# Optimization experiments

Measured on AMD Instinct MI355X. Metric: run time of the kernel, lower is better.

The kernel has to match this reference:

```python
import jax, jax.numpy as jnp
import numpy as np

N_PATCHES = 14
PS = 16            # patch size: 224 / 14
C, H_IMG, W_IMG = 3, 224, 224
HIDDEN = 768
HEADS = 12
DH = HIDDEN // HEADS
BLOCKS = 12
MLP = 4 * HIDDEN
OUT = 1000
SEQ = N_PATCHES ** 2 + 1  # 197
BATCH = 64


def get_positional_embeddings(seq_len, d):
    # sin(i/10000^(j/d)) for even j, cos(i/10000^((j-1)/d)) for odd j
    i = jnp.arange(seq_len, dtype=jnp.float32)[:, None]
    j = jnp.arange(d)[None, :]
    even = (j % 2 == 0)
    expo = jnp.where(even, j, j - 1).astype(jnp.float32) / d
    ang = i / (10000.0 ** expo)
    return jnp.where(even, jnp.sin(ang), jnp.cos(ang))


def layernorm(x, g, b, eps=1e-5):
    mu = x.mean(-1, keepdims=True)
    var = ((x - mu) ** 2).mean(-1, keepdims=True)
    return (x - mu) / jnp.sqrt(var + eps) * g + b


def mhsa(x, qw, qb, kw, kb, vw, vb):
    # x: [B,S,HIDDEN]; per-head linears qw/kw/vw: [H,DH,DH] (torch Linear weight layout)
    B, S, _ = x.shape
    xh = x.reshape(B, S, HEADS, DH)
    q = jnp.einsum('bshd,hed->bshe', xh, qw) + qb
    k = jnp.einsum('bshd,hed->bshe', xh, kw) + kb
    v = jnp.einsum('bshd,hed->bshe', xh, vw) + vb
    scores = jnp.einsum('bshe,bthe->bhst', q, k) / jnp.sqrt(jnp.float32(DH))
    attn = jax.nn.softmax(scores, axis=-1)
    out = jnp.einsum('bhst,bthe->bshe', attn, v)
    return out.reshape(B, S, HIDDEN)


def vit_block(x, p):
    ln1_g, ln1_b, qw, qb, kw, kb, vw, vb, ln2_g, ln2_b, w1, b1, w2, b2 = p
    x = x + mhsa(layernorm(x, ln1_g, ln1_b), qw, qb, kw, kb, vw, vb)
    h = layernorm(x, ln2_g, ln2_b)
    h = jax.nn.gelu(h @ w1.T + b1, approximate=False) @ w2.T + b2
    return x + h


def patchify(images):
    # [N,C,H,W] -> [N, n_patches^2, C*PS*PS], channel-major within each patch
    n = images.shape[0]
    x = images.reshape(n, C, N_PATCHES, PS, N_PATCHES, PS)
    x = x.transpose(0, 2, 4, 1, 3, 5)  # n, pi, pj, c, ps, ps
    return x.reshape(n, N_PATCHES * N_PATCHES, C * PS * PS)


def setup_inputs() -> dict:
    key = jax.random.key(0)
    ks = jax.random.split(key, 20)
    s = 0.02
    return {
        'images': jax.random.normal(ks[0], (BATCH, C, H_IMG, W_IMG), jnp.float32),
        'mapper_w': jax.random.normal(ks[1], (HIDDEN, C * PS * PS), jnp.float32) * s,
        'mapper_b': jnp.zeros((HIDDEN,), jnp.float32),
        'cls_token': jax.random.uniform(ks[2], (1, HIDDEN), jnp.float32),
        'ln1_g': jnp.ones((BLOCKS, HIDDEN), jnp.float32),
        'ln1_b': jnp.zeros((BLOCKS, HIDDEN), jnp.float32),
        'qw': jax.random.normal(ks[3], (BLOCKS, HEADS, DH, DH), jnp.float32) * s,
        'qb': jnp.zeros((BLOCKS, HEADS, DH), jnp.float32),
        'kw': jax.random.normal(ks[4], (BLOCKS, HEADS, DH, DH), jnp.float32) * s,
        'kb': jnp.zeros((BLOCKS, HEADS, DH), jnp.float32),
        'vw': jax.random.normal(ks[5], (BLOCKS, HEADS, DH, DH), jnp.float32) * s,
        'vb': jnp.zeros((BLOCKS, HEADS, DH), jnp.float32),
        'ln2_g': jnp.ones((BLOCKS, HIDDEN), jnp.float32),
        'ln2_b': jnp.zeros((BLOCKS, HIDDEN), jnp.float32),
        'w1': jax.random.normal(ks[6], (BLOCKS, MLP, HIDDEN), jnp.float32) * s,
        'b1': jnp.zeros((BLOCKS, MLP), jnp.float32),
        'w2': jax.random.normal(ks[7], (BLOCKS, HIDDEN, MLP), jnp.float32) * s,
        'b2': jnp.zeros((BLOCKS, HIDDEN), jnp.float32),
        'head_w': jax.random.normal(ks[8], (OUT, HIDDEN), jnp.float32) * s,
        'head_b': jnp.zeros((OUT,), jnp.float32),
    }


def reference(images, mapper_w, mapper_b, cls_token, ln1_g, ln1_b, qw, qb, kw, kb,
              vw, vb, ln2_g, ln2_b, w1, b1, w2, b2, head_w, head_b):
    n = images.shape[0]
    patches = patchify(images)
    tokens = patches @ mapper_w.T + mapper_b                      # [B, 196, HIDDEN]
    cls = jnp.broadcast_to(cls_token[None], (n, 1, HIDDEN))
    tokens = jnp.concatenate([cls, tokens], axis=1)               # [B, 197, HIDDEN]
    out = tokens + get_positional_embeddings(SEQ, HIDDEN)[None]

    stacked = (ln1_g, ln1_b, qw, qb, kw, kb, vw, vb, ln2_g, ln2_b, w1, b1, w2, b2)

    def step(x, p):
        return vit_block(x, p), None

    out, _ = jax.lax.scan(step, out, stacked)
    cls_out = out[:, 0]                                           # [B, HIDDEN]
    return jax.nn.softmax(cls_out @ head_w.T + head_b, axis=-1)
```

## Files before the change

kernel.cpp:

```cpp
#include <hip/hip_runtime.h>
#include <cstdint>
#include <cstddef>
#include <cstdio>

using u16 = unsigned short;
using u32 = unsigned int;

typedef __attribute__((ext_vector_type(8))) __bf16 bf16x8;
typedef __attribute__((ext_vector_type(4))) float f32x4;

struct alignas(16) U128 { u32 w[4]; };
struct alignas(16) F4   { float x[4]; };
struct alignas(8)  US4  { u16 h[4]; };

#define DEVFN static __device__ __forceinline__

DEVFN u16 f2bf(float x) {
  union { float f; u32 u; } v; v.f = x;
  u32 r = v.u + 0x7fffu + ((v.u >> 16) & 1u);
  return (u16)(r >> 16);
}

DEVFN bf16x8 ld16(const u16* p) { return __builtin_bit_cast(bf16x8, *(const U128*)p); }

DEVFN f32x4 mfma16(bf16x8 a, bf16x8 b, f32x4 c) {
  return __builtin_amdgcn_mfma_f32_16x16x32_bf16(a, b, c, 0, 0, 0);
}

DEVFN void gload_lds16(const u16* g, u16* l) {
  __builtin_amdgcn_global_load_lds(
      (const __attribute__((address_space(1))) void*)g,
      (__attribute__((address_space(3))) void*)l, 16, 0, 0);
}

DEVFN float gelu(float x) {
  float z = fabsf(x) * 0.70710678118f;
  float t = __builtin_amdgcn_rcpf(1.f + 0.3275911f * z);
  float p = t * (0.254829592f + t * (-0.284496736f + t * (1.421413741f +
            t * (-1.453152027f + t * 1.061405429f))));
  float e = __expf(-z * z);
  float erfz = 1.f - p * e;
  erfz = copysignf(erfz, x);
  return 0.5f * x * (1.f + erfz);
}

DEVFN void remap_bid(int bid, int Mb, int Nb, int& bm, int& bn) {
  const int ngrp  = Mb >> 3;
  const int per   = Nb << 3;
  const int nfull = ngrp * per;
  if (bid < nfull) {
    const int bmg = bid / per;
    const int rem = bid - bmg * per;
    bn = rem >> 3;
    bm = (bmg << 3) + (rem & 7);
  } else {
    const int r = bid - nfull;
    const int q = r / Nb;
    bm = (ngrp << 3) + q;
    bn = r - q * Nb;
  }
}

constexpr int SEQL   = 197;
constexpr int NB     = 64;
constexpr int NH     = 12;
constexpr int MROWS  = NB * SEQL;
constexpr int MPAD   = 12672;
constexpr int MPAD2  = 12800;
constexpr int MPATCH = NB * 196;
constexpr int SP     = 208;
constexpr int SP2    = 224;
constexpr int BHN    = NB * NH;

constexpr int QSZ    = 2304 * 128;
constexpr int WSZ    = 3072 * 768;

constexpr size_t OFF_X    = 0;
constexpr size_t OFF_ALN  = OFF_X    + (size_t)MPAD * 768 * 4;
constexpr size_t OFF_H    = OFF_ALN  + (size_t)MPAD2 * 768 * 2;
constexpr size_t OFF_WMAP = OFF_H    + (size_t)MPAD2 * 3072 * 2;
constexpr size_t OFF_Q    = OFF_WMAP + (size_t)768 * 768 * 2;
constexpr size_t OFF_K    = OFF_Q    + (size_t)BHN * SP * 64 * 2;
constexpr size_t OFF_VT   = OFF_K    + (size_t)BHN * SP * 64 * 2;
constexpr size_t OFF_PAT  = OFF_VT   + (size_t)BHN * 64 * SP2 * 2;
constexpr size_t OFF_POS  = OFF_PAT  + (size_t)MPATCH * 768 * 2;
constexpr size_t OFF_WTS  = OFF_POS  + (size_t)SEQL * 768 * 4;
constexpr size_t WS_SMALL = OFF_WTS + (size_t)(QSZ + 2 * WSZ) * 2;
constexpr size_t WS_BIG   = OFF_WTS + (size_t)12 * (QSZ + 2 * WSZ) * 2;

__global__ void zero_kernel(u32* __restrict__ p, long n) {
  long i = (long)blockIdx.x * 256 + threadIdx.x;
  long stride = (long)gridDim.x * 256;
  for (; i < n; i += stride) p[i] = 0u;
}

__global__ void padzero_kernel(u16* __restrict__ Q, u16* __restrict__ Kp,
                               u16* __restrict__ Vt) {
  const int NQ32 = BHN * 352;
  const int NV   = BHN * 64 * 27;
  int i = blockIdx.x * 256 + threadIdx.x;
  if (i < NQ32) {
    int bh = i / 352, r = i - bh * 352;
    ((u32*)(Q + ((size_t)bh * SP + 197) * 64))[r] = 0u;
  } else if (i < 2 * NQ32) {
    int j = i - NQ32;
    int bh = j / 352, r = j - bh * 352;
    ((u32*)(Kp + ((size_t)bh * SP + 197) * 64))[r] = 0u;
  } else if (i < 2 * NQ32 + NV) {
    int j = i - 2 * NQ32;
    int be = j / 27, s = j - be * 27;
    Vt[(size_t)be * SP2 + 197 + s] = 0;
  }
}

__global__ void cvt_kernel(const float* __restrict__ src, u16* __restrict__ dst, int n) {
  int i = blockIdx.x * 256 + threadIdx.x;
  if (i < n) dst[i] = f2bf(src[i]);
}

__global__ void pos_kernel(float* __restrict__ pos) {
  int i = blockIdx.x * 256 + threadIdx.x;
  if (i >= SEQL * 768) return;
  int s = i / 768, j = i - s * 768;
  float expo = (float)(j & ~1) * (1.0f / 768.0f);
  float ang  = (float)s * expf(-expo * logf(10000.0f));
  pos[i] = (j & 1) ? cosf(ang) : sinf(ang);
}

__global__ void cls_kernel(const float* __restrict__ cls, const float* __restrict__ pos,
                           float* __restrict__ X) {
  int b = blockIdx.x;
  for (int c = threadIdx.x; c < 768; c += 256)
    X[(size_t)b * SEQL * 768 + c] = cls[c] + pos[c];
}

__global__ void patchify_kernel(const float* __restrict__ img, u16* __restrict__ out) {
  int i = blockIdx.x * 256 + threadIdx.x;
  if (i >= MPATCH * 768) return;
  int m = i / 768, k = i - m * 768;
  int b = m / 196, p = m - b * 196;
  int py = p / 14, px = p - py * 14;
  int c = k >> 8, rem = k & 255, iy = rem >> 4, ix = rem & 15;
  float v = img[(((size_t)b * 3 + c) * 224 + py * 16 + iy) * 224 + px * 16 + ix];
  out[i] = f2bf(v);
}

__global__ void prep_all(const float* __restrict__ qw, const float* __restrict__ kw,
                         const float* __restrict__ vw, const float* __restrict__ w1,
                         const float* __restrict__ w2,
                         u16* __restrict__ Wq, u16* __restrict__ W1b,
                         u16* __restrict__ W2b) {
  const int NQ = 12 * QSZ;
  const int NV = 12 * (WSZ / 4);
  int i = blockIdx.x * 256 + threadIdx.x;
  if (i < NQ) {
    int blk = i / QSZ;
    int r = i - blk * QSZ;
    int n = r >> 7, kk = r & 127;
    int p = n / 768, ef = n - p * 768;
    int h = ef >> 6, e = ef & 63;
    float v = 0.f;
    if ((kk >> 6) == (h & 1)) {
      int d = kk & 63;
      const float* w = (p == 0) ? qw : (p == 1) ? kw : vw;
      v = w[(((size_t)blk * NH + h) * 64 + e) * 64 + d];
    }
    Wq[i] = f2bf(v);
  } else if (i < NQ + NV) {
    int j = (i - NQ) * 4;
    F4 v = *(const F4*)(w1 + j);
    US4 o;
    #pragma unroll
    for (int r = 0; r < 4; ++r) o.h[r] = f2bf(v.x[r]);
    *(US4*)(W1b + j) = o;
  } else if (i < NQ + 2 * NV) {
    int j = (i - NQ - NV) * 4;
    F4 v = *(const F4*)(w2 + j);
    US4 o;
    #pragma unroll
    for (int r = 0; r < 4; ++r) o.h[r] = f2bf(v.x[r]);
    *(US4*)(W2b + j) = o;
  }
}

__global__ void prep_kernel(const float* __restrict__ qw, const float* __restrict__ kw,
                            const float* __restrict__ vw, const float* __restrict__ w1,
                            const float* __restrict__ w2,
                            u16* __restrict__ Wqkv, u16* __restrict__ W1b,
                            u16* __restrict__ W2b, int blk) {
  const int NV = WSZ / 4;
  int i = blockIdx.x * 256 + threadIdx.x;
  if (i < QSZ) {
    int n = i >> 7, kk = i & 127;
    int p = n / 768, ef = n - p * 768;
    int h = ef >> 6, e = ef & 63;
    float v = 0.f;
    if ((kk >> 6) == (h & 1)) {
      int d = kk & 63;
      const float* w = (p == 0) ? qw : (p == 1) ? kw : vw;
      v = w[(((size_t)blk * NH + h) * 64 + e) * 64 + d];
    }
    Wqkv[i] = f2bf(v);
  } else if (i < QSZ + NV) {
    int j = (i - QSZ) * 4;
    F4 v = *(const F4*)(w1 + (size_t)blk * WSZ + j);
    US4 o;
    #pragma unroll
    for (int r = 0; r < 4; ++r) o.h[r] = f2bf(v.x[r]);
    *(US4*)(W1b + j) = o;
  } else if (i < QSZ + 2 * NV) {
    int j = (i - QSZ - NV) * 4;
    F4 v = *(const F4*)(w2 + (size_t)blk * WSZ + j);
    US4 o;
    #pragma unroll
    for (int r = 0; r < 4; ++r) o.h[r] = f2bf(v.x[r]);
    *(US4*)(W2b + j) = o;
  }
}

__global__ __launch_bounds__(256) void ln_kernel(const float* __restrict__ X,
    const float* __restrict__ g, const float* __restrict__ b, u16* __restrict__ out) {
  int row  = blockIdx.x * 4 + (threadIdx.x >> 6);
  int lane = threadIdx.x & 63;
  const float* x = X + (size_t)row * 768 + lane * 12;
  F4 a0 = *(const F4*)(x);
  F4 a1 = *(const F4*)(x + 4);
  F4 a2 = *(const F4*)(x + 8);
  float v[12];
  #pragma unroll
  for (int j = 0; j < 4; ++j) { v[j] = a0.x[j]; v[4 + j] = a1.x[j]; v[8 + j] = a2.x[j]; }
  float s = 0.f, q = 0.f;
  #pragma unroll
  for (int j = 0; j < 12; ++j) { s += v[j]; q += v[j] * v[j]; }
  #pragma unroll
  for (int d = 1; d < 64; d <<= 1) { s += __shfl_xor(s, d); q += __shfl_xor(q, d); }
  float mu  = s * (1.f / 768.f);
  float var = q * (1.f / 768.f) - mu * mu;
  float rs  = rsqrtf(var + 1e-5f);
  const float* gp = g + lane * 12;
  const float* bp = b + lane * 12;
  u16* op = out + (size_t)row * 768 + lane * 12;
  u16 o[12];
  #pragma unroll
  for (int j = 0; j < 12; ++j) o[j] = f2bf((v[j] - mu) * rs * gp[j] + bp[j]);
  #pragma unroll
  for (int c = 0; c < 3; ++c) {
    US4 w; w.h[0] = o[c*4]; w.h[1] = o[c*4+1]; w.h[2] = o[c*4+2]; w.h[3] = o[c*4+3];
    *(US4*)(op + c * 4) = w;
  }
}

enum { EPI_PATCH = 0, EPI_QKV = 1, EPI_GELU = 2, EPI_RESID = 3 };

template<int EPI>
__global__ __launch_bounds__(256, 3) void gemm128(
    const u16* __restrict__ A, const u16* __restrict__ B, int K, int lda, int ldb,
    int Mb, int Nb,
    const float* __restrict__ e0, const float* __restrict__ e1, const float* __restrict__ e2,
    float* __restrict__ f0, const float* __restrict__ f1,
    u16* __restrict__ o0, u16* __restrict__ o1, u16* __restrict__ o2) {
  __shared__ u16 Ab[3][128 * 32];
  __shared__ u16 Bb[3][128 * 32];
  const int tid  = threadIdx.x;
  const int wave = tid >> 6, lane = tid & 63;
  int bm, bn;
  remap_bid(blockIdx.x, Mb, Nb, bm, bn);
  const int fr = lane & 15, fg = lane >> 4;
  const int srow = wave * 16 + (lane >> 2);
  const int gcol = ((lane & 3) ^ ((lane >> 3) & 3)) * 8;
  const u16* gA = A + (size_t)(bm * 128 + srow) * lda + gcol;
  const u16* gB = B + (size_t)(bn * 128 + srow) * ldb + gcol;
  const int wm = (wave >> 1) * 64, wn = (wave & 1) * 64;
  const int sl = (fg ^ ((fr >> 1) & 3)) * 8;
  const int nt = K >> 5;

  auto STAGE = [&](int c, int t) {
    gload_lds16(gA + t * 32,                    &Ab[c][0] + wave * 512);
    gload_lds16(gA + t * 32 + (size_t)64 * lda, &Ab[c][0] + wave * 512 + 2048);
    gload_lds16(gB + t * 32,                    &Bb[c][0] + wave * 512);
    gload_lds16(gB + t * 32 + (size_t)64 * ldb, &Bb[c][0] + wave * 512 + 2048);
  };

  f32x4 acc[4][4] = {};
  STAGE(0, 0);
  if (nt > 1) STAGE(1, 1);
  int bi = 0;
  for (int t = 0; t < nt; ++t) {
    if (t + 1 < nt) asm volatile("s_waitcnt vmcnt(4)" ::: "memory");
    else            asm volatile("s_waitcnt vmcnt(0)" ::: "memory");
    __builtin_amdgcn_s_barrier();
    if (t + 2 < nt) { int si = bi + 2; if (si >= 3) si -= 3; STAGE(si, t + 2); }
    const u16* ab   = &Ab[bi][0];
    const u16* bbuf = &Bb[bi][0];
    bf16x8 af[4], bfv[4];
    #pragma unroll
    for (int i = 0; i < 4; ++i) af[i]  = ld16(ab + (wm + i * 16 + fr) * 32 + sl);
    #pragma unroll
    for (int j = 0; j < 4; ++j) bfv[j] = ld16(bbuf + (wn + j * 16 + fr) * 32 + sl);
    __builtin_amdgcn_s_setprio(1);
    #pragma unroll
    for (int i = 0; i < 4; ++i)
      #pragma unroll
      for (int j = 0; j < 4; ++j)
        acc[i][j] = mfma16(af[i], bfv[j], acc[i][j]);
    __builtin_amdgcn_s_setprio(0);
    bi = (bi + 1 == 3) ? 0 : bi + 1;
  }

  #pragma unroll
  for (int i = 0; i < 4; ++i) {
    #pragma unroll
    for (int r = 0; r < 4; ++r) {
      const int m = bm * 128 + wm + i * 16 + fg * 4 + r;
      if constexpr (EPI == EPI_PATCH) {
        const int bb = m / 196;
        const int s  = m - bb * 196 + 1;
        float* xrow = f0 + ((size_t)bb * SEQL + s) * 768;
        const float* prow = f1 + (size_t)s * 768;
        #pragma unroll
        for (int j = 0; j < 4; ++j) {
          const int n = bn * 128 + wn + j * 16 + fr;
          xrow[n] = acc[i][j][r] + e0[n] + prow[n];
        }
      } else {
        if (m < MROWS) {
          float* xrow = f0 + (size_t)m * 768;
          #pragma unroll
          for (int j = 0; j < 4; ++j) {
            const int n = bn * 128 + wn + j * 16 + fr;
            xrow[n] += acc[i][j][r] + e0[n];
          }
        }
      }
    }
  }
}

__global__ __launch_bounds__(256, 3) void gemm128f_gelu(
    const u16* __restrict__ A, const u16* __restrict__ B,
    const float* __restrict__ e0, u16* __restrict__ o0,
    int ntiles, int nblocks) {
  __shared__ u16 Ab[3][128 * 32];
  __shared__ u16 Bb[3][128 * 32];
  constexpr int lda = 768, ldb = 768, nt = 24;
  const int tid = threadIdx.x, wave = tid >> 6, lane = tid & 63;
  const int fr = lane & 15, fg = lane >> 4;
  const int srow = wave * 16 + (lane >> 2);
  const int gcol = ((lane & 3) ^ ((lane >> 3) & 3)) * 8;
  const int wm = (wave >> 1) * 64, wn = (wave & 1) * 64;
  const int sl = (fg ^ ((fr >> 1) & 3)) * 8;
  const int myTiles = (ntiles - (int)blockIdx.x + nblocks - 1) / nblocks;
  const int total = myTiles * nt;

  int s_t  = blockIdx.x;
  int s_kk = 0;
  const u16 *s_gA, *s_gB;
  {
    int bm, bn; remap_bid(s_t, 99, 24, bm, bn);
    s_gA = A + (size_t)(bm * 128 + srow) * lda + gcol;
    s_gB = B + (size_t)(bn * 128 + srow) * ldb + gcol;
  }
  auto STAGE1 = [&](int c) {
    gload_lds16(s_gA + s_kk * 32,                    &Ab[c][0] + wave * 512);
    gload_lds16(s_gA + s_kk * 32 + (size_t)64 * lda, &Ab[c][0] + wave * 512 + 2048);
    gload_lds16(s_gB + s_kk * 32,                    &Bb[c][0] + wave * 512);
    gload_lds16(s_gB + s_kk * 32 + (size_t)64 * ldb, &Bb[c][0] + wave * 512 + 2048);
    if (++s_kk == nt) {
      s_kk = 0;
      s_t += nblocks;
      if (s_t < ntiles) {
        int bm, bn; remap_bid(s_t, 99, 24, bm, bn);
        s_gA = A + (size_t)(bm * 128 + srow) * lda + gcol;
        s_gB = B + (size_t)(bn * 128 + srow) * ldb + gcol;
      }
    }
  };

  STAGE1(0);
  if (total > 1) STAGE1(1);
  int bi = 0, g = 0;
  for (int t = blockIdx.x; t < ntiles; t += nblocks) {
    int bm, bn; remap_bid(t, 99, 24, bm, bn);
    f32x4 acc[4][4] = {};
    for (int k = 0; k < nt; ++k, ++g) {
      if (g + 1 < total) asm volatile("s_waitcnt vmcnt(4)" ::: "memory");
      else               asm volatile("s_waitcnt vmcnt(0)" ::: "memory");
      __builtin_amdgcn_s_barrier();
      if (g + 2 < total) { int si = bi + 2; if (si >= 3) si -= 3; STAGE1(si); }
      const u16* ab   = &Ab[bi][0];
      const u16* bbuf = &Bb[bi][0];
      bf16x8 af[4], bfv[4];
      #pragma unroll
      for (int i = 0; i < 4; ++i) af[i]  = ld16(ab + (wm + i * 16 + fr) * 32 + sl);
      #pragma unroll
      for (int j = 0; j < 4; ++j) bfv[j] = ld16(bbuf + (wn + j * 16 + fr) * 32 + sl);
      __builtin_amdgcn_s_setprio(1);
      #pragma unroll
      for (int i = 0; i < 4; ++i)
        #pragma unroll
        for (int j = 0; j < 4; ++j)
          acc[i][j] = mfma16(af[i], bfv[j], acc[i][j]);
      __builtin_amdgcn_s_setprio(0);
      bi = (bi + 1 == 3) ? 0 : bi + 1;
    }
    #pragma unroll
    for (int i = 0; i < 4; ++i) {
      #pragma unroll
      for (int r = 0; r < 4; ++r) {
        const int m = bm * 128 + wm + i * 16 + fg * 4 + r;
        u16* hrow = o0 + (size_t)m * 3072;
        #pragma unroll
        for (int j = 0; j < 4; ++j) {
          const int n = bn * 128 + wn + j * 16 + fr;
          hrow[n] = f2bf(gelu(acc[i][j][r] + e0[n]));
        }
      }
    }
  }
}

__global__ __launch_bounds__(256, 2) void qkv_gemm(
    const u16* __restrict__ A, const u16* __restrict__ B,
    const float* __restrict__ e0, const float* __restrict__ e1, const float* __restrict__ e2,
    u16* __restrict__ o0, u16* __restrict__ o1, u16* __restrict__ o2) {
  __shared__ u16 Ab[4][128 * 32];
  __shared__ u16 Bb[4][128 * 32];
  const int tid = threadIdx.x, wave = tid >> 6, lane = tid & 63;
  int bm, bn;
  remap_bid(blockIdx.x, MPAD / 128, 18, bm, bn);
  const int fr = lane & 15, fg = lane >> 4;
  const u16* Aw = A + (bn % 6) * 128;
  const int srow = wave * 16 + (lane >> 2);
  const int gcol = ((lane & 3) ^ ((lane >> 3) & 3)) * 8;
  const u16* gA = Aw + (size_t)(bm * 128 + srow) * 768 + gcol;
  const u16* gB = B + (size_t)(bn * 128 + srow) * 128 + gcol;
  const int wm = (wave >> 1) * 64, wn = (wave & 1) * 64;
  const int sl = (fg ^ ((fr >> 1) & 3)) * 8;

  #pragma unroll
  for (int c = 0; c < 4; ++c) {
    gload_lds16(gA + c * 32,                    &Ab[c][0] + wave * 512);
    gload_lds16(gA + c * 32 + (size_t)64 * 768, &Ab[c][0] + wave * 512 + 2048);
    gload_lds16(gB + c * 32,                    &Bb[c][0] + wave * 512);
    gload_lds16(gB + c * 32 + (size_t)64 * 128, &Bb[c][0] + wave * 512 + 2048);
  }
  asm volatile("s_waitcnt vmcnt(0)" ::: "memory");
  __builtin_amdgcn_s_barrier();

  f32x4 acc[4][4] = {};
  #pragma unroll
  for (int c = 0; c < 4; ++c) {
    bf16x8 af[4], bfv[4];
    #pragma unroll
    for (int i = 0; i < 4; ++i) af[i]  = ld16(&Ab[c][0] + (wm + i * 16 + fr) * 32 + sl);
    #pragma unroll
    for (int j = 0; j < 4; ++j) bfv[j] = ld16(&Bb[c][0] + (wn + j * 16 + fr) * 32 + sl);
    __builtin_amdgcn_s_setprio(1);
    #pragma unroll
    for (int i = 0; i < 4; ++i)
      #pragma unroll
      for (int j = 0; j < 4; ++j)
        acc[i][j] = mfma16(af[i], bfv[j], acc[i][j]);
    __builtin_amdgcn_s_setprio(0);
  }

  #pragma unroll
  for (int i = 0; i < 4; ++i) {
    #pragma unroll
    for (int r = 0; r < 4; ++r) {
      const int m = bm * 128 + wm + i * 16 + fg * 4 + r;
      if (m < MROWS) {
        const int bb = m / 197;
        const int s  = m - bb * 197;
        #pragma unroll
        for (int j = 0; j < 4; ++j) {
          const int n = bn * 128 + wn + j * 16 + fr;
          const int p = n / 768;
          const int ef = n - p * 768;
          const int h = ef >> 6, e = ef & 63;
          const size_t bh = (size_t)bb * NH + h;
          if (p == 0)      o0[(bh * SP + s) * 64 + e] = f2bf((acc[i][j][r] + e0[ef]) * 0.125f);
          else if (p == 1) o1[(bh * SP + s) * 64 + e] = f2bf(acc[i][j][r] + e1[ef]);
          else             o2[(bh * 64 + e) * SP2 + s] = f2bf(acc[i][j][r] + e2[ef]);
        }
      }
    }
  }
}

__global__ __launch_bounds__(256, 2) void attn_kernel(const u16* __restrict__ Q,
    const u16* __restrict__ Km, const u16* __restrict__ Vt, float* __restrict__ X) {
  __shared__ u16  P[4][16 * SP2];
  __shared__ u16  Kl[208 * 72];
  __shared__ float sums[4][16];
  const int bh = blockIdx.x;
  const int b = bh / NH, h = bh - b * NH;
  const int wave = threadIdx.x >> 6, lane = threadIdx.x & 63;
  const int fr = lane & 15, fg = lane >> 4;
  const u16* Qb = Q  + (size_t)bh * SP * 64;
  const u16* Kb = Km + (size_t)bh * SP * 64;
  const u16* Vb = Vt + (size_t)bh * 64 * SP2;
  {
    const int r0 = threadIdx.x >> 2;
    const int e  = (threadIdx.x & 3) * 16;
    #pragma unroll
    for (int rr = r0; rr < 208; rr += 64)
      *(U128*)(Kl + rr * 72 + e) = *(const U128*)(Kb + (size_t)rr * 64 + e);
  }
  __syncthreads();
  u16* Pl = &P[wave][0];
  for (int qt = wave; qt < 13; qt += 4) {
    const int s0 = qt * 16;
    bf16x8 qf0 = ld16(Qb + (size_t)(s0 + fr) * 64 + fg * 8);
    bf16x8 qf1 = ld16(Qb + (size_t)(s0 + fr) * 64 + 32 + fg * 8);
    f32x4 sc[13];
    #pragma unroll
    for (int tf = 0; tf < 13; ++tf) {
      f32x4 a = {0.f, 0.f, 0.f, 0.f};
      bf16x8 k0 = ld16(Kl + (tf * 16 + fr) * 72 + fg * 8);
      bf16x8 k1 = ld16(Kl + (tf * 16 + fr) * 72 + 32 + fg * 8);
      a = mfma16(qf0, k0, a);
      a = mfma16(qf1, k1, a);
      sc[tf] = a;
    }
    float mx[4] = {-3e38f, -3e38f, -3e38f, -3e38f};
    #pragma unroll
    for (int tf = 0; tf < 13; ++tf) {
      const bool ok = (tf * 16 + fr) < 197;
      #pragma unroll
      for (int r = 0; r < 4; ++r) {
        float v = ok ? sc[tf][r] : -3e38f;
        sc[tf][r] = v;
        mx[r] = fmaxf(mx[r], v);
      }
    }
    #pragma unroll
    for (int r = 0; r < 4; ++r)
      #pragma unroll
      for (int d = 1; d < 16; d <<= 1) mx[r] = fmaxf(mx[r], __shfl_xor(mx[r], d));
    float sm[4] = {0.f, 0.f, 0.f, 0.f};
    #pragma unroll
    for (int tf = 0; tf < 13; ++tf) {
      #pragma unroll
      for (int r = 0; r < 4; ++r) {
        float e = __expf(sc[tf][r] - mx[r]);
        sm[r] += e;
        Pl[(fg * 4 + r) * SP2 + tf * 16 + fr] = f2bf(e);
      }
    }
    #pragma unroll
    for (int r = 0; r < 4; ++r) {
      #pragma unroll
      for (int d = 1; d < 16; d <<= 1) sm[r] += __shfl_xor(sm[r], d);
      if (fr == 0) sums[wave][fg * 4 + r] = sm[r];
    }
    #pragma unroll
    for (int r = 0; r < 4; ++r) Pl[(fg * 4 + r) * SP2 + 208 + fr] = 0;
    f32x4 o[4] = {};
    #pragma unroll
    for (int ks = 0; ks < 7; ++ks) {
      bf16x8 pf = ld16(Pl + fr * SP2 + ks * 32 + fg * 8);
      #pragma unroll
      for (int ef = 0; ef < 4; ++ef) {
        bf16x8 vf = ld16(Vb + (size_t)(ef * 16 + fr) * SP2 + ks * 32 + fg * 8);
        o[ef] = mfma16(vf, pf, o[ef]);
      }
    }
    const float inv = 1.f / sums[wave][fr];
    const int s = s0 + fr;
    if (s < 197) {
      float* xp = X + ((size_t)b * SEQL + s) * 768 + h * 64;
      #pragma unroll
      for (int ef = 0; ef < 4; ++ef)
        #pragma unroll
        for (int r = 0; r < 4; ++r)
          xp[ef * 16 + fg * 4 + r] += o[ef][r] * inv;
    }
  }
}

__global__ __launch_bounds__(256) void head_kernel(const float* __restrict__ X,
    const float* __restrict__ hw, const float* __restrict__ hb, float* __restrict__ out) {
  __shared__ float xr[768];
  __shared__ float lg[1000];
  __shared__ float red[8];
  const int b = blockIdx.x, tid = threadIdx.x;
  for (int c = tid; c < 768; c += 256) xr[c] = X[(size_t)b * SEQL * 768 + c];
  __syncthreads();
  for (int n = tid; n < 1000; n += 256) {
    const F4* w4 = (const F4*)(hw + (size_t)n * 768);
    const F4* x4 = (const F4*)xr;
    float acc = hb[n];
    for (int k = 0; k < 192; ++k) {
      F4 w = w4[k]; F4 xv = x4[k];
      acc += w.x[0] * xv.x[0] + w.x[1] * xv.x[1] + w.x[2] * xv.x[2] + w.x[3] * xv.x[3];
    }
    lg[n] = acc;
  }
  __syncthreads();
  float m = -3e38f;
  for (int n = tid; n < 1000; n += 256) m = fmaxf(m, lg[n]);
  #pragma unroll
  for (int d = 1; d < 64; d <<= 1) m = fmaxf(m, __shfl_xor(m, d));
  if ((tid & 63) == 0) red[tid >> 6] = m;
  __syncthreads();
  m = fmaxf(fmaxf(red[0], red[1]), fmaxf(red[2], red[3]));
  float s = 0.f;
  for (int n = tid; n < 1000; n += 256) s += expf(lg[n] - m);
  #pragma unroll
  for (int d = 1; d < 64; d <<= 1) s += __shfl_xor(s, d);
  if ((tid & 63) == 0) red[4 + (tid >> 6)] = s;
  __syncthreads();
  s = red[4] + red[5] + red[6] + red[7];
  const float inv = 1.f / s;
  for (int n = tid; n < 1000; n += 256) out[(size_t)b * 1000 + n] = expf(lg[n] - m) * inv;
}

extern "C" void kernel_launch(void* const* d_in, const int* in_sizes, int n_in,
                              void* d_out, int out_size, void* d_ws, size_t ws_size,
                              hipStream_t stream) {
  (void)in_sizes; (void)n_in; (void)out_size;
  if (ws_size < WS_SMALL) { printf("ws too small: %zu < %zu\n", ws_size, WS_SMALL); return; }
  const bool hoist = ws_size >= WS_BIG;

  const float* images   = (const float*)d_in[0];
  const float* mapper_w = (const float*)d_in[1];
  const float* mapper_b = (const float*)d_in[2];
  const float* cls_tok  = (const float*)d_in[3];
  const float* ln1_g    = (const float*)d_in[4];
  const float* ln1_b    = (const float*)d_in[5];
  const float* qw       = (const float*)d_in[6];
  const float* qb       = (const float*)d_in[7];
  const float* kw       = (const float*)d_in[8];
  const float* kb       = (const float*)d_in[9];
  const float* vw       = (const float*)d_in[10];
  const float* vb       = (const float*)d_in[11];
  const float* ln2_g    = (const float*)d_in[12];
  const float* ln2_b    = (const float*)d_in[13];
  const float* w1       = (const float*)d_in[14];
  const float* b1       = (const float*)d_in[15];
  const float* w2       = (const float*)d_in[16];
  const float* b2       = (const float*)d_in[17];
  const float* head_w   = (const float*)d_in[18];
  const float* head_b   = (const float*)d_in[19];

  char* ws = (char*)d_ws;
  float* X    = (float*)(ws + OFF_X);
  u16*  Aln   = (u16*)(ws + OFF_ALN);
  u16*  Hb    = (u16*)(ws + OFF_H);
  u16*  Wmap  = (u16*)(ws + OFF_WMAP);
  u16*  Qb    = (u16*)(ws + OFF_Q);
  u16*  Kb    = (u16*)(ws + OFF_K);
  u16*  Vtb   = (u16*)(ws + OFF_VT);
  u16*  Pat   = (u16*)(ws + OFF_PAT);
  float* Pos  = (float*)(ws + OFF_POS);
  u16*  WqA   = (u16*)(ws + OFF_WTS);
  u16*  W1A   = WqA + (size_t)(hoist ? 12 : 1) * QSZ;
  u16*  W2A   = W1A + (size_t)(hoist ? 12 : 1) * WSZ;

  padzero_kernel<<<(2 * BHN * 352 + BHN * 64 * 27 + 255) / 256, 256, 0, stream>>>(Qb, Kb, Vtb);
  zero_kernel<<<64, 256, 0, stream>>>((u32*)(X + (size_t)MROWS * 768), (long)((MPAD - MROWS) * 768));

  pos_kernel<<<(SEQL * 768 + 255) / 256, 256, 0, stream>>>(Pos);
  cvt_kernel<<<(768 * 768 + 255) / 256, 256, 0, stream>>>(mapper_w, Wmap, 768 * 768);
  patchify_kernel<<<(MPATCH * 768 + 255) / 256, 256, 0, stream>>>(images, Pat);
  cls_kernel<<<NB, 256, 0, stream>>>(cls_tok, Pos, X);

  if (hoist) {
    const int N_ALL = 12 * QSZ + 2 * 12 * (WSZ / 4);
    prep_all<<<(N_ALL + 255) / 256, 256, 0, stream>>>(qw, kw, vw, w1, w2, WqA, W1A, W2A);
  }

  gemm128<EPI_PATCH><<<(MPATCH / 128) * (768 / 128), 256, 0, stream>>>(
      Pat, Wmap, 768, 768, 768, MPATCH / 128, 768 / 128,
      mapper_b, nullptr, nullptr, X, Pos, nullptr, nullptr, nullptr);

  const int PREP_N = QSZ + 2 * (WSZ / 4);
  for (int blk = 0; blk < 12; ++blk) {
    u16* Wq_b = WqA + (size_t)(hoist ? blk : 0) * QSZ;
    u16* W1_b = W1A + (size_t)(hoist ? blk : 0) * WSZ;
    u16* W2_b = W2A + (size_t)(hoist ? blk : 0) * WSZ;
    ln_kernel<<<MPAD / 4, 256, 0, stream>>>(X, ln1_g + blk * 768, ln1_b + blk * 768, Aln);
    if (!hoist)
      prep_kernel<<<(PREP_N + 255) / 256, 256, 0, stream>>>(
          qw, kw, vw, w1, w2, Wq_b, W1_b, W2_b, blk);
    qkv_gemm<<<(MPAD / 128) * 18, 256, 0, stream>>>(
        Aln, Wq_b, qb + blk * 768, kb + blk * 768, vb + blk * 768, Qb, Kb, Vtb);
    attn_kernel<<<BHN, 256, 0, stream>>>(Qb, Kb, Vtb, X);
    ln_kernel<<<MPAD / 4, 256, 0, stream>>>(X, ln2_g + blk * 768, ln2_b + blk * 768, Aln);
    gemm128f_gelu<<<768, 256, 0, stream>>>(Aln, W1_b, b1 + blk * 3072, Hb, 2376, 768);
    gemm128<EPI_RESID><<<(MPAD / 128) * (768 / 128), 256, 0, stream>>>(
        Hb, W2_b, 3072, 3072, 3072, MPAD / 128, 768 / 128,
        b2 + blk * 768, nullptr, nullptr, X, nullptr, nullptr, nullptr, nullptr);
  }

  head_kernel<<<NB, 256, 0, stream>>>(X, head_w, head_b, (float*)d_out);
}
```

Measured before the change: 4.107 ms.

## Make QKV GEMM persistent with triple-buffered cross-tile pipelined loads

The per-tile QKV GEMM, which loaded all four K-chunks and then computed, becomes a persistent kernel over 768 blocks. Each block walks several output tiles, and a 3-stage LDS ring prefetches chunks across tile boundaries so global loads overlap MFMA work and epilogue stores. LDS use drops from 4 to 3 buffers per operand and launch bounds rise to 3 blocks per CU for occupancy. The cost is more barriers per tile and a fixed grid that may leave some blocks with an uneven number of tiles.

```diff
diff --git a/kernel.cpp b/kernel.cpp
--- a/kernel.cpp
+++ b/kernel.cpp
@@ -419,69 +419,95 @@
   }
 }
 
-__global__ __launch_bounds__(256, 2) void qkv_gemm(
+__global__ __launch_bounds__(256, 3) void qkv_flat(
     const u16* __restrict__ A, const u16* __restrict__ B,
     const float* __restrict__ e0, const float* __restrict__ e1, const float* __restrict__ e2,
-    u16* __restrict__ o0, u16* __restrict__ o1, u16* __restrict__ o2) {
-  __shared__ u16 Ab[4][128 * 32];
-  __shared__ u16 Bb[4][128 * 32];
+    u16* __restrict__ o0, u16* __restrict__ o1, u16* __restrict__ o2,
+    int ntiles, int nblocks) {
+  __shared__ u16 Ab[3][128 * 32];
+  __shared__ u16 Bb[3][128 * 32];
+  constexpr int lda = 768, ldb = 128, nt = 4;
   const int tid = threadIdx.x, wave = tid >> 6, lane = tid & 63;
-  int bm, bn;
-  remap_bid(blockIdx.x, MPAD / 128, 18, bm, bn);
   const int fr = lane & 15, fg = lane >> 4;
-  const u16* Aw = A + (bn % 6) * 128;
   const int srow = wave * 16 + (lane >> 2);
   const int gcol = ((lane & 3) ^ ((lane >> 3) & 3)) * 8;
-  const u16* gA = Aw + (size_t)(bm * 128 + srow) * 768 + gcol;
-  const u16* gB = B + (size_t)(bn * 128 + srow) * 128 + gcol;
   const int wm = (wave >> 1) * 64, wn = (wave & 1) * 64;
   const int sl = (fg ^ ((fr >> 1) & 3)) * 8;
-
-  #pragma unroll
-  for (int c = 0; c < 4; ++c) {
-    gload_lds16(gA + c * 32,                    &Ab[c][0] + wave * 512);
-    gload_lds16(gA + c * 32 + (size_t)64 * 768, &Ab[c][0] + wave * 512 + 2048);
-    gload_lds16(gB + c * 32,                    &Bb[c][0] + wave * 512);
-    gload_lds16(gB + c * 32 + (size_t)64 * 128, &Bb[c][0] + wave * 512 + 2048);
-  }
-  asm volatile("s_waitcnt vmcnt(0)" ::: "memory");
-  __builtin_amdgcn_s_barrier();
-
-  f32x4 acc[4][4] = {};
-  #pragma unroll
-  for (int c = 0; c < 4; ++c) {
-    bf16x8 af[4], bfv[4];
-    #pragma unroll
-    for (int i = 0; i < 4; ++i) af[i]  = ld16(&Ab[c][0] + (wm + i * 16 + fr) * 32 + sl);
-    #pragma unroll
-    for (int j = 0; j < 4; ++j) bfv[j] = ld16(&Bb[c][0] + (wn + j * 16 + fr) * 32 + sl);
-    __builtin_amdgcn_s_setprio(1);
-    #pragma unroll
-    for (int i = 0; i < 4; ++i)
-      #pragma unroll
-      for (int j = 0; j < 4; ++j)
-        acc[i][j] = mfma16(af[i], bfv[j], acc[i][j]);
-    __builtin_amdgcn_s_setprio(0);
-  }
-
-  #pragma unroll
-  for (int i = 0; i < 4; ++i) {
-    #pragma unroll
-    for (int r = 0; r < 4; ++r) {
-      const int m = bm * 128 + wm + i * 16 + fg * 4 + r;
-      if (m < MROWS) {
-        const int bb = m / 197;
-        const int s  = m - bb * 197;
+  const int myTiles = (ntiles - (int)blockIdx.x + nblocks - 1) / nblocks;
+  if (myTiles <= 0) return;
+  const int total = myTiles * nt;
+
+  int s_t  = blockIdx.x;
+  int s_kk = 0;
+  const u16 *s_gA, *s_gB;
+  {
+    int bm, bn; remap_bid(s_t, 99, 18, bm, bn);
+    s_gA = A + (bn % 6) * 128 + (size_t)(bm * 128 + srow) * lda + gcol;
+    s_gB = B + (size_t)(bn * 128 + srow) * ldb + gcol;
+  }
+  auto STAGE1 = [&](int c) {
+    gload_lds16(s_gA + s_kk * 32,                    &Ab[c][0] + wave * 512);
+    gload_lds16(s_gA + s_kk * 32 + (size_t)64 * lda, &Ab[c][0] + wave * 512 + 2048);
+    gload_lds16(s_gB + s_kk * 32,                    &Bb[c][0] + wave * 512);
+    gload_lds16(s_gB + s_kk * 32 + (size_t)64 * ldb, &Bb[c][0] + wave * 512 + 2048);
+    if (++s_kk == nt) {
+      s_kk = 0;
+      s_t += nblocks;
+      if (s_t < ntiles) {
+        int bm, bn; remap_bid(s_t, 99, 18, bm, bn);
+        s_gA = A + (bn % 6) * 128 + (size_t)(bm * 128 + srow) * lda + gcol;
+        s_gB = B + (size_t)(bn * 128 + srow) * ldb + gcol;
+      }
+    }
+  };
+
+  STAGE1(0);
+  if (total > 1) STAGE1(1);
+  int bi = 0, g = 0;
+  for (int t = blockIdx.x; t < ntiles; t += nblocks) {
+    int bm, bn; remap_bid(t, 99, 18, bm, bn);
+    f32x4 acc[4][4] = {};
+    #pragma unroll
+    for (int k = 0; k < nt; ++k, ++g) {
+      if (g + 1 < total) asm volatile("s_waitcnt vmcnt(4)" ::: "memory");
+      else               asm volatile("s_waitcnt vmcnt(0)" ::: "memory");
+      __builtin_amdgcn_s_barrier();
+      if (g + 2 < total) { int si = bi + 2; if (si >= 3) si -= 3; STAGE1(si); }
+      const u16* ab   = &Ab[bi][0];
+      const u16* bbuf = &Bb[bi][0];
+      bf16x8 af[4], bfv[4];
+      #pragma unroll
+      for (int i = 0; i < 4; ++i) af[i]  = ld16(ab + (wm + i * 16 + fr) * 32 + sl);
+      #pragma unroll
+      for (int j = 0; j < 4; ++j) bfv[j] = ld16(bbuf + (wn + j * 16 + fr) * 32 + sl);
+      __builtin_amdgcn_s_setprio(1);
+      #pragma unroll
+      for (int i = 0; i < 4; ++i)
         #pragma unroll
-        for (int j = 0; j < 4; ++j) {
-          const int n = bn * 128 + wn + j * 16 + fr;
-          const int p = n / 768;
-          const int ef = n - p * 768;
-          const int h = ef >> 6, e = ef & 63;
-          const size_t bh = (size_t)bb * NH + h;
-          if (p == 0)      o0[(bh * SP + s) * 64 + e] = f2bf((acc[i][j][r] + e0[ef]) * 0.125f);
-          else if (p == 1) o1[(bh * SP + s) * 64 + e] = f2bf(acc[i][j][r] + e1[ef]);
-          else             o2[(bh * 64 + e) * SP2 + s] = f2bf(acc[i][j][r] + e2[ef]);
+        for (int j = 0; j < 4; ++j)
+          acc[i][j] = mfma16(af[i], bfv[j], acc[i][j]);
+      __builtin_amdgcn_s_setprio(0);
+      bi = (bi + 1 == 3) ? 0 : bi + 1;
+    }
+    #pragma unroll
+    for (int i = 0; i < 4; ++i) {
+      #pragma unroll
+      for (int r = 0; r < 4; ++r) {
+        const int m = bm * 128 + wm + i * 16 + fg * 4 + r;
+        if (m < MROWS) {
+          const int bb = m / 197;
+          const int s  = m - bb * 197;
+          #pragma unroll
+          for (int j = 0; j < 4; ++j) {
+            const int n = bn * 128 + wn + j * 16 + fr;
+            const int p = n / 768;
+            const int ef = n - p * 768;
+            const int h = ef >> 6, e = ef & 63;
+            const size_t bh = (size_t)bb * NH + h;
+            if (p == 0)      o0[(bh * SP + s) * 64 + e] = f2bf((acc[i][j][r] + e0[ef]) * 0.125f);
+            else if (p == 1) o1[(bh * SP + s) * 64 + e] = f2bf(acc[i][j][r] + e1[ef]);
+            else             o2[(bh * 64 + e) * SP2 + s] = f2bf(acc[i][j][r] + e2[ef]);
+          }
         }
       }
     }
@@ -684,8 +710,9 @@
     if (!hoist)
       prep_kernel<<<(PREP_N + 255) / 256, 256, 0, stream>>>(
           qw, kw, vw, w1, w2, Wq_b, W1_b, W2_b, blk);
-    qkv_gemm<<<(MPAD / 128) * 18, 256, 0, stream>>>(
-        Aln, Wq_b, qb + blk * 768, kb + blk * 768, vb + blk * 768, Qb, Kb, Vtb);
+    qkv_flat<<<768, 256, 0, stream>>>(
+        Aln, Wq_b, qb + blk * 768, kb + blk * 768, vb + blk * 768,
+        Qb, Kb, Vtb, (MPAD / 128) * 18, 768);
     attn_kernel<<<BHN, 256, 0, stream>>>(Qb, Kb, Vtb, X);
     ln_kernel<<<MPAD / 4, 256, 0, stream>>>(X, ln2_g + blk * 768, ln2_b + blk * 768, Aln);
     gemm128f_gelu<<<768, 256, 0, stream>>>(Aln, W1_b, b1 + blk * 3072, Hb, 2376, 768);
```

After: 3.959 ms (median of 3 runs). -3.6%, faster.

## Use 256x256 tiled 8-wave GEMM for MLP layers and persistent QKV GEMM

Applied to the files above, without the earlier changes.

Replaces the 128x128 MLP GEMMs (FC1 with GELU, FC2 with residual) with a new 256x256-tile, 512-thread kernel using K=64 double-buffered LDS. Loads for the next stage are interleaved between four MFMA phases separated by barriers. The QKV projection becomes a persistent, triple-buffered kernel reusing the old flat-GELU pipeline. The goal is higher arithmetic intensity and better latency hiding. In exchange it needs a larger M padding (MPAD2) with extra zeroing of Aln and Hb rows, and fewer blocks for the small FC2 GEMM.

```diff
diff --git a/kernel.cpp b/kernel.cpp
--- a/kernel.cpp
+++ b/kernel.cpp
@@ -336,13 +336,129 @@
   }
 }
 
-__global__ __launch_bounds__(256, 3) void gemm128f_gelu(
+template<int MG, int KK>
+DEVFN void phase_mfma(const u16* ab, const u16* bbuf, int wr, int wc, int fr, int fg,
+                      f32x4 (&acc)[8][4], bf16x8 (&bf)[4], bool loadB) {
+  bf16x8 af[4];
+  #pragma unroll
+  for (int a = 0; a < 4; ++a) {
+    const int row = wr * 128 + (MG * 4 + a) * 16 + fr;
+    af[a] = ld16(ab + row * 64 + (((KK * 4 + fg) ^ (row & 7)) * 8));
+  }
+  if (loadB) {
+    #pragma unroll
+    for (int nf = 0; nf < 4; ++nf) {
+      const int row = wc * 64 + nf * 16 + fr;
+      bf[nf] = ld16(bbuf + row * 64 + (((KK * 4 + fg) ^ (row & 7)) * 8));
+    }
+  }
+  __builtin_amdgcn_s_setprio(1);
+  #pragma unroll
+  for (int a = 0; a < 4; ++a)
+    #pragma unroll
+    for (int nf = 0; nf < 4; ++nf)
+      acc[MG * 4 + a][nf] = mfma16(af[a], bf[nf], acc[MG * 4 + a][nf]);
+  __builtin_amdgcn_s_setprio(0);
+}
+
+template<int EPI>
+__global__ __launch_bounds__(512, 2) void gemm256p(
+    const u16* __restrict__ A, const u16* __restrict__ B, int K, int Mb, int Nb,
+    const float* __restrict__ e0, float* __restrict__ f0, u16* __restrict__ o0) {
+  __shared__ u16 Ab[2][256 * 64];
+  __shared__ u16 Bb[2][256 * 64];
+  const int tid = threadIdx.x;
+  const int wid = tid >> 6, lane = tid & 63;
+  const int fr = lane & 15, fg = lane >> 4;
+  const int wr = wid >> 2, wc = wid & 3;
+  int bm, bn;
+  remap_bid(blockIdx.x, Mb, Nb, bm, bn);
+  const int nt = K >> 6;
+
+  const int r0 = tid >> 3,        c0 = tid & 7;
+  const int r1 = (512 + tid) >> 3, c1 = (512 + tid) & 7;
+  const int gc0 = ((c0 ^ (r0 & 7)) * 8);
+  const int gc1 = ((c1 ^ (r1 & 7)) * 8);
+  const int d0 = (wid * 64) * 8;
+  const int d1 = (512 + wid * 64) * 8;
+
+  auto STAGE_A = [&](int b_, int h, int t) {
+    const u16* g0 = A + (size_t)(bm * 256 + h * 128 + r0) * K + t * 64 + gc0;
+    const u16* g1 = A + (size_t)(bm * 256 + h * 128 + r1) * K + t * 64 + gc1;
+    u16* base = &Ab[b_][0] + h * 8192;
+    gload_lds16(g0, base + d0);
+    gload_lds16(g1, base + d1);
+  };
+  auto STAGE_B = [&](int b_, int h, int t) {
+    const u16* g0 = B + (size_t)(bn * 256 + h * 128 + r0) * K + t * 64 + gc0;
+    const u16* g1 = B + (size_t)(bn * 256 + h * 128 + r1) * K + t * 64 + gc1;
+    u16* base = &Bb[b_][0] + h * 8192;
+    gload_lds16(g0, base + d0);
+    gload_lds16(g1, base + d1);
+  };
+
+  f32x4 acc[8][4] = {};
+
+  STAGE_A(0, 0, 0); STAGE_A(0, 1, 0); STAGE_B(0, 0, 0); STAGE_B(0, 1, 0);
+  asm volatile("s_waitcnt vmcnt(0)" ::: "memory");
+  __builtin_amdgcn_s_barrier();
+
+  for (int t = 0; t < nt; ++t) {
+    const int cb = t & 1, nb2 = cb ^ 1;
+    const bool pf = (t + 1 < nt);
+    const u16* ab   = &Ab[cb][0];
+    const u16* bbuf = &Bb[cb][0];
+    bf16x8 bf[4];
+    if (pf) { STAGE_A(nb2, 0, t + 1); asm volatile("s_waitcnt vmcnt(2)" ::: "memory"); }
+    else    { asm volatile("s_waitcnt vmcnt(0)" ::: "memory"); }
+    __builtin_amdgcn_s_barrier();
+    phase_mfma<0, 0>(ab, bbuf, wr, wc, fr, fg, acc, bf, true);
+    __builtin_amdgcn_s_barrier();
+    if (pf) STAGE_A(nb2, 1, t + 1);
+    phase_mfma<1, 0>(ab, bbuf, wr, wc, fr, fg, acc, bf, false);
+    __builtin_amdgcn_s_barrier();
+    if (pf) STAGE_B(nb2, 0, t + 1);
+    phase_mfma<0, 1>(ab, bbuf, wr, wc, fr, fg, acc, bf, true);
+    __builtin_amdgcn_s_barrier();
+    if (pf) STAGE_B(nb2, 1, t + 1);
+    phase_mfma<1, 1>(ab, bbuf, wr, wc, fr, fg, acc, bf, false);
+    __builtin_amdgcn_s_barrier();
+  }
+
+  #pragma unroll
+  for (int mf = 0; mf < 8; ++mf) {
+    #pragma unroll
+    for (int r = 0; r < 4; ++r) {
+      const int m = bm * 256 + wr * 128 + mf * 16 + fg * 4 + r;
+      if constexpr (EPI == EPI_GELU) {
+        u16* hrow = o0 + (size_t)m * 3072;
+        #pragma unroll
+        for (int nf = 0; nf < 4; ++nf) {
+          const int n = bn * 256 + wc * 64 + nf * 16 + fr;
+          hrow[n] = f2bf(gelu(acc[mf][nf][r] + e0[n]));
+        }
+      } else {
+        if (m < MROWS) {
+          float* xrow = f0 + (size_t)m * 768;
+          #pragma unroll
+          for (int nf = 0; nf < 4; ++nf) {
+            const int n = bn * 256 + wc * 64 + nf * 16 + fr;
+            xrow[n] += acc[mf][nf][r] + e0[n];
+          }
+        }
+      }
+    }
+  }
+}
+
+__global__ __launch_bounds__(256, 3) void qkv_flat(
     const u16* __restrict__ A, const u16* __restrict__ B,
-    const float* __restrict__ e0, u16* __restrict__ o0,
+    const float* __restrict__ e0, const float* __restrict__ e1, const float* __restrict__ e2,
+    u16* __restrict__ o0, u16* __restrict__ o1, u16* __restrict__ o2,
     int ntiles, int nblocks) {
   __shared__ u16 Ab[3][128 * 32];
   __shared__ u16 Bb[3][128 * 32];
-  constexpr int lda = 768, ldb = 768, nt = 24;
+  constexpr int lda = 768, ldb = 128, nt = 4;
   const int tid = threadIdx.x, wave = tid >> 6, lane = tid & 63;
   const int fr = lane & 15, fg = lane >> 4;
   const int srow = wave * 16 + (lane >> 2);
@@ -350,14 +466,15 @@
   const int wm = (wave >> 1) * 64, wn = (wave & 1) * 64;
   const int sl = (fg ^ ((fr >> 1) & 3)) * 8;
   const int myTiles = (ntiles - (int)blockIdx.x + nblocks - 1) / nblocks;
+  if (myTiles <= 0) return;
   const int total = myTiles * nt;
 
   int s_t  = blockIdx.x;
   int s_kk = 0;
   const u16 *s_gA, *s_gB;
   {
-    int bm, bn; remap_bid(s_t, 99, 24, bm, bn);
-    s_gA = A + (size_t)(bm * 128 + srow) * lda + gcol;
+    int bm, bn; remap_bid(s_t, 99, 18, bm, bn);
+    s_gA = A + (bn % 6) * 128 + (size_t)(bm * 128 + srow) * lda + gcol;
     s_gB = B + (size_t)(bn * 128 + srow) * ldb + gcol;
   }
   auto STAGE1 = [&](int c) {
@@ -369,8 +486,8 @@
       s_kk = 0;
       s_t += nblocks;
       if (s_t < ntiles) {
-        int bm, bn; remap_bid(s_t, 99, 24, bm, bn);
-        s_gA = A + (size_t)(bm * 128 + srow) * lda + gcol;
+        int bm, bn; remap_bid(s_t, 99, 18, bm, bn);
+        s_gA = A + (bn % 6) * 128 + (size_t)(bm * 128 + srow) * lda + gcol;
         s_gB = B + (size_t)(bn * 128 + srow) * ldb + gcol;
       }
     }
@@ -380,8 +497,9 @@
   if (total > 1) STAGE1(1);
   int bi = 0, g = 0;
   for (int t = blockIdx.x; t < ntiles; t += nblocks) {
-    int bm, bn; remap_bid(t, 99, 24, bm, bn);
+    int bm, bn; remap_bid(t, 99, 18, bm, bn);
     f32x4 acc[4][4] = {};
+    #pragma unroll
     for (int k = 0; k < nt; ++k, ++g) {
       if (g + 1 < total) asm volatile("s_waitcnt vmcnt(4)" ::: "memory");
       else               asm volatile("s_waitcnt vmcnt(0)" ::: "memory");
@@ -408,80 +526,20 @@
       #pragma unroll
       for (int r = 0; r < 4; ++r) {
         const int m = bm * 128 + wm + i * 16 + fg * 4 + r;
-        u16* hrow = o0 + (size_t)m * 3072;
-        #pragma unroll
-        for (int j = 0; j < 4; ++j) {
-          const int n = bn * 128 + wn + j * 16 + fr;
-          hrow[n] = f2bf(gelu(acc[i][j][r] + e0[n]));
-        }
-      }
-    }
-  }
-}
-
-__global__ __launch_bounds__(256, 2) void qkv_gemm(
-    const u16* __restrict__ A, const u16* __restrict__ B,
-    const float* __restrict__ e0, const float* __restrict__ e1, const float* __restrict__ e2,
-    u16* __restrict__ o0, u16* __restrict__ o1, u16* __restrict__ o2) {
-  __shared__ u16 Ab[4][128 * 32];
-  __shared__ u16 Bb[4][128 * 32];
-  const int tid = threadIdx.x, wave = tid >> 6, lane = tid & 63;
-  int bm, bn;
-  remap_bid(blockIdx.x, MPAD / 128, 18, bm, bn);
-  const int fr = lane & 15, fg = lane >> 4;
-  const u16* Aw = A + (bn % 6) * 128;
-  const int srow = wave * 16 + (lane >> 2);
-  const int gcol = ((lane & 3) ^ ((lane >> 3) & 3)) * 8;
-  const u16* gA = Aw + (size_t)(bm * 128 + srow) * 768 + gcol;
-  const u16* gB = B + (size_t)(bn * 128 + srow) * 128 + gcol;
-  const int wm = (wave >> 1) * 64, wn = (wave & 1) * 64;
-  const int sl = (fg ^ ((fr >> 1) & 3)) * 8;
-
-  #pragma unroll
-  for (int c = 0; c < 4; ++c) {
-    gload_lds16(gA + c * 32,                    &Ab[c][0] + wave * 512);
-    gload_lds16(gA + c * 32 + (size_t)64 * 768, &Ab[c][0] + wave * 512 + 2048);
-    gload_lds16(gB + c * 32,                    &Bb[c][0] + wave * 512);
-    gload_lds16(gB + c * 32 + (size_t)64 * 128, &Bb[c][0] + wave * 512 + 2048);
-  }
-  asm volatile("s_waitcnt vmcnt(0)" ::: "memory");
-  __builtin_amdgcn_s_barrier();
-
-  f32x4 acc[4][4] = {};
-  #pragma unroll
-  for (int c = 0; c < 4; ++c) {
-    bf16x8 af[4], bfv[4];
-    #pragma unroll
-    for (int i = 0; i < 4; ++i) af[i]  = ld16(&Ab[c][0] + (wm + i * 16 + fr) * 32 + sl);
-    #pragma unroll
-    for (int j = 0; j < 4; ++j) bfv[j] = ld16(&Bb[c][0] + (wn + j * 16 + fr) * 32 + sl);
-    __builtin_amdgcn_s_setprio(1);
-    #pragma unroll
-    for (int i = 0; i < 4; ++i)
-      #pragma unroll
-      for (int j = 0; j < 4; ++j)
-        acc[i][j] = mfma16(af[i], bfv[j], acc[i][j]);
-    __builtin_amdgcn_s_setprio(0);
-  }
-
-  #pragma unroll
-  for (int i = 0; i < 4; ++i) {
-    #pragma unroll
-    for (int r = 0; r < 4; ++r) {
-      const int m = bm * 128 + wm + i * 16 + fg * 4 + r;
-      if (m < MROWS) {
-        const int bb = m / 197;
-        const int s  = m - bb * 197;
-        #pragma unroll
-        for (int j = 0; j < 4; ++j) {
-          const int n = bn * 128 + wn + j * 16 + fr;
-          const int p = n / 768;
-          const int ef = n - p * 768;
-          const int h = ef >> 6, e = ef & 63;
-          const size_t bh = (size_t)bb * NH + h;
-          if (p == 0)      o0[(bh * SP + s) * 64 + e] = f2bf((acc[i][j][r] + e0[ef]) * 0.125f);
-          else if (p == 1) o1[(bh * SP + s) * 64 + e] = f2bf(acc[i][j][r] + e1[ef]);
-          else             o2[(bh * 64 + e) * SP2 + s] = f2bf(acc[i][j][r] + e2[ef]);
+        if (m < MROWS) {
+          const int bb = m / 197;
+          const int s  = m - bb * 197;
+          #pragma unroll
+          for (int j = 0; j < 4; ++j) {
+            const int n = bn * 128 + wn + j * 16 + fr;
+            const int p = n / 768;
+            const int ef = n - p * 768;
+            const int h = ef >> 6, e = ef & 63;
+            const size_t bh = (size_t)bb * NH + h;
+            if (p == 0)      o0[(bh * SP + s) * 64 + e] = f2bf((acc[i][j][r] + e0[ef]) * 0.125f);
+            else if (p == 1) o1[(bh * SP + s) * 64 + e] = f2bf(acc[i][j][r] + e1[ef]);
+            else             o2[(bh * 64 + e) * SP2 + s] = f2bf(acc[i][j][r] + e2[ef]);
+          }
         }
       }
     }
@@ -660,6 +718,7 @@
 
   padzero_kernel<<<(2 * BHN * 352 + BHN * 64 * 27 + 255) / 256, 256, 0, stream>>>(Qb, Kb, Vtb);
   zero_kernel<<<64, 256, 0, stream>>>((u32*)(X + (size_t)MROWS * 768), (long)((MPAD - MROWS) * 768));
+  zero_kernel<<<192, 256, 0, stream>>>((u32*)(Aln + (size_t)MPAD * 768), (long)((MPAD2 - MPAD) * 768 / 2));
 
   pos_kernel<<<(SEQL * 768 + 255) / 256, 256, 0, stream>>>(Pos);
   cvt_kernel<<<(768 * 768 + 255) / 256, 256, 0, stream>>>(mapper_w, Wmap, 768 * 768);
@@ -684,14 +743,15 @@
     if (!hoist)
       prep_kernel<<<(PREP_N + 255) / 256, 256, 0, stream>>>(
           qw, kw, vw, w1, w2, Wq_b, W1_b, W2_b, blk);
-    qkv_gemm<<<(MPAD / 128) * 18, 256, 0, stream>>>(
-        Aln, Wq_b, qb + blk * 768, kb + blk * 768, vb + blk * 768, Qb, Kb, Vtb);
+    qkv_flat<<<768, 256, 0, stream>>>(
+        Aln, Wq_b, qb + blk * 768, kb + blk * 768, vb + blk * 768,
+        Qb, Kb, Vtb, (MPAD / 128) * 18, 768);
     attn_kernel<<<BHN, 256, 0, stream>>>(Qb, Kb, Vtb, X);
     ln_kernel<<<MPAD / 4, 256, 0, stream>>>(X, ln2_g + blk * 768, ln2_b + blk * 768, Aln);
-    gemm128f_gelu<<<768, 256, 0, stream>>>(Aln, W1_b, b1 + blk * 3072, Hb, 2376, 768);
-    gemm128<EPI_RESID><<<(MPAD / 128) * (768 / 128), 256, 0, stream>>>(
-        Hb, W2_b, 3072, 3072, 3072, MPAD / 128, 768 / 128,
-        b2 + blk * 768, nullptr, nullptr, X, nullptr, nullptr, nullptr, nullptr);
+    gemm256p<EPI_GELU><<<(MPAD2 / 256) * (3072 / 256), 512, 0, stream>>>(
+        Aln, W1_b, 768, MPAD2 / 256, 3072 / 256, b1 + blk * 3072, nullptr, Hb);
+    gemm256p<EPI_RESID><<<(MPAD2 / 256) * (768 / 256), 512, 0, stream>>>(
+        Hb, W2_b, 3072, MPAD2 / 256, 768 / 256, b2 + blk * 768, X, nullptr);
   }
 
   head_kernel<<<NB, 256, 0, stream>>>(X, head_w, head_b, (float*)d_out);
```

Result: slower. 4.928 ms (+20.0%).
